# Kernel optimization log

Measured on AMD Instinct MI355X. Metric: run time of the kernel, lower is better.

Reference implementation:

```python
import jax, jax.numpy as jnp
import numpy as np

WIN, SIGMA = 11, 1.5
C1, C2, EPS = 0.01 ** 2, 0.03 ** 2, 1e-8


def _gauss_window(win=WIN, sigma=SIGMA):
    coords = jnp.arange(win, dtype=jnp.float32) - (win - 1) / 2
    g = jnp.exp(-coords ** 2 / (2 * sigma ** 2))
    g = g / g.sum()
    return (g[:, None] * g[None, :])[None, None, :, :]


def setup_inputs() -> dict:
    key = jax.random.key(0)
    k1, k2 = jax.random.split(key)
    N, C, H, W = 32, 1, 512, 512
    x = jax.random.uniform(k1, (N, C, H, W), dtype=jnp.float32)
    y = jax.random.uniform(k2, (N, C, H, W), dtype=jnp.float32)
    w = _gauss_window()
    return {"x": x, "y": y, "w": w}


def _conv(x, w):
    pad = w.shape[-1] // 2
    return jax.lax.conv_general_dilated(
        x, w, window_strides=(1, 1), padding=[(pad, pad), (pad, pad)],
        dimension_numbers=("NCHW", "OIHW", "NCHW"))


def reference(x, y, w):
    w = w.astype(x.dtype)
    n = x.shape[0]
    # One fused conv over all five planes stacked on the batch dim.
    stacked = jnp.concatenate([x, y, x * x, y * y, x * y], axis=0)
    conv = _conv(stacked, w)
    mu_x, mu_y, ex2, ey2, exy = (conv[i * n:(i + 1) * n] for i in range(5))
    mu_x2, mu_y2, mu_xy = mu_x ** 2, mu_y ** 2, mu_x * mu_y
    sig_x2 = ex2 - mu_x2
    sig_y2 = ey2 - mu_y2
    sig_xy = exy - mu_xy
    num = (2 * mu_xy + C1) * (2 * sig_xy + C2)
    den = (mu_x2 + mu_y2 + C1) * (sig_x2 + sig_y2 + C2)
    return jnp.clip(num / (den + EPS), 0.0, 1.0).mean()
```

## Files before the change

### kernel.cpp

```cpp
#include <hip/hip_runtime.h>


typedef float v2f __attribute__((ext_vector_type(2)));
typedef float v4f __attribute__((ext_vector_type(4)));

#define IMG_H 512
#define IMG_W 512
#define NIMG  32
#define NT    256
#define RROWS 32
#define ITERS (RROWS + 10)
#define LDSW  524

#define C1F  1.0e-4f
#define C2F  9.0e-4f
#define EPSF 1.0e-8f

static __device__ __forceinline__ v2f pkfma(float s, v2f a, v2f b) {
    v2f sv = {s, s};
    return __builtin_elementwise_fma(sv, a, b);
}

__global__ __launch_bounds__(NT) void ssim_kernel(
    const float* __restrict__ xg, const float* __restrict__ yg,
    const float* __restrict__ wg, float* __restrict__ out)
{
    const int t    = threadIdx.x;
    const int lane = t & 63;
    const int chnk = blockIdx.x;
    const int img  = blockIdx.y;
    const int r0   = chnk * RROWS;
    const int c0   = 2 * t;

    const float* xb = xg + (size_t)img * (IMG_H * IMG_W);
    const float* yb = yg + (size_t)img * (IMG_H * IMG_W);

    __shared__ alignas(16) v2f ssd[2][LDSW];
    __shared__ float wredS[4];

    float rs = 0.f;
    if (lane < 11) {
        #pragma unroll
        for (int j = 0; j < 11; ++j) rs += wg[lane * 11 + j];
    }
    float g[11];
    #pragma unroll
    for (int k = 0; k < 11; ++k) {
        int gi = __shfl(__float_as_int(rs), k, 64);
        g[k] = __int_as_float(__builtin_amdgcn_readfirstlane(gi));
    }

    const v2f z2 = {0.f, 0.f};

    if (t < 5)        { ssd[0][1 + t]   = z2; ssd[1][1 + t]   = z2; }
    else if (t < 10)  { ssd[0][513 + t] = z2; ssd[1][513 + t] = z2; }

    v2f rSD[11][2], rQ[11][2];

    v2f pfx, pfy;
    {
        const int r = r0 - 5;
        if ((unsigned)r < IMG_H) {
            pfx = *(const v2f*)(xb + (size_t)r * IMG_W + c0);
            pfy = *(const v2f*)(yb + (size_t)r * IMG_W + c0);
        } else { pfx = z2; pfy = z2; }
    }

    float acc = 0.f;

    for (int ii = 0; ii < 44; ii += 11) {
        #pragma unroll
        for (int s = 0; s < 11; ++s) {
            const int i = ii + s;
            if (i < ITERS) {
                const int pb = i & 1;
                {
                    const v2f sv = pfx + pfy;
                    const v2f dv = pfx - pfy;
                    v4f st = {sv.x, dv.x, sv.y, dv.y};
                    *(v4f*)&ssd[pb][6 + c0] = st;
                }
                __syncthreads();

                {
                    const int r = r0 - 4 + i;
                    if ((unsigned)r < IMG_H) {
                        pfx = *(const v2f*)(xb + (size_t)r * IMG_W + c0);
                        pfy = *(const v2f*)(yb + (size_t)r * IMG_W + c0);
                    } else { pfx = z2; pfy = z2; }
                }

                v2f hA = z2, hB = z2, qA = z2, qB = z2;
                #pragma unroll
                for (int m = 0; m < 7; ++m) {
                    const v4f w4 = *(const v4f*)&ssd[pb][c0 + 2 * m];
                    const v2f e0 = {w4.x, w4.y};
                    const v2f e1 = {w4.z, w4.w};
                    {
                        const int j = 2 * m;
                        if (j >= 1) {
                            const v2f f0 = e0 * e0;
                            if (j <= 11) {
                                hA = pkfma(g[j - 1], e0, hA);
                                qA = pkfma(g[j - 1], f0, qA);
                            }
                            if (j >= 2) {
                                hB = pkfma(g[j - 2], e0, hB);
                                qB = pkfma(g[j - 2], f0, qB);
                            }
                        }
                    }
                    {
                        const int j = 2 * m + 1;
                        if (j <= 12) {
                            const v2f f1 = e1 * e1;
                            if (j <= 11) {
                                hA = pkfma(g[j - 1], e1, hA);
                                qA = pkfma(g[j - 1], f1, qA);
                            }
                            if (j >= 2) {
                                hB = pkfma(g[j - 2], e1, hB);
                                qB = pkfma(g[j - 2], f1, qB);
                            }
                        }
                    }
                }
                rSD[s][0] = hA; rSD[s][1] = hB;
                rQ[s][0]  = qA; rQ[s][1]  = qB;

                if (i >= 10) {
                    #pragma unroll
                    for (int c = 0; c < 2; ++c) {
                        v2f mSD = z2, mQ = z2;
                        #pragma unroll
                        for (int j = 0; j < 11; ++j) {
                            const int sl = (s + 1 + j) % 11;
                            mSD = pkfma(g[j], rSD[sl][c], mSD);
                            mQ  = pkfma(g[j], rQ[sl][c],  mQ);
                        }
                        const v2f t2 = mSD * mSD;
                        const float a    = 0.5f  * (t2.x + t2.y);
                        const float muxy = 0.25f * (t2.x - t2.y);
                        const float ep   = 0.5f  * (mQ.x + mQ.y);
                        const float eq   = 0.25f * (mQ.x - mQ.y);
                        const float sxy  = eq - muxy;
                        const float ssum = ep - a;
                        const float num  = fmaf(2.f, muxy, C1F) * fmaf(2.f, sxy, C2F);
                        const float den  = (a + C1F) * (ssum + C2F);
                        float v = num * __builtin_amdgcn_rcpf(den + EPSF);
                        acc += fminf(fmaxf(v, 0.f), 1.f);
                    }
                }
            }
        }
    }

    #pragma unroll
    for (int off = 32; off > 0; off >>= 1)
        acc += __shfl_down(acc, off, 64);
    __syncthreads();
    if (lane == 0) wredS[t >> 6] = acc;
    __syncthreads();
    if (t == 0) {
        const float tot = (wredS[0] + wredS[1]) + (wredS[2] + wredS[3]);
        atomicAdd(out, tot * (1.0f / (float)((size_t)NIMG * IMG_H * IMG_W)));
    }
}

extern "C" void kernel_launch(void* const* d_in, const int* in_sizes, int n_in,
                              void* d_out, int out_size, void* d_ws, size_t ws_size,
                              hipStream_t stream) {
    const float* x = (const float*)d_in[0];
    const float* y = (const float*)d_in[1];
    const float* w = (const float*)d_in[2];
    float* out = (float*)d_out;

    hipMemsetAsync(out, 0, sizeof(float), stream);

    dim3 grid(IMG_H / RROWS, NIMG);
    ssim_kernel<<<grid, dim3(NT), 0, stream>>>(x, y, w, out);
}
```

Baseline: 118.9 us.

## Batch eleven rows per LDS stage to cut block barriers

The LDS staging buffer grows from two rows to eleven. Each thread now loads eleven input rows into registers at once, writes them all to LDS, then runs eleven horizontal/vertical filter steps before the next barrier. This replaces one barrier per row with two per eleven-row chunk and puts more global loads in flight at a time. The cost is more LDS (about 46KB per block), more registers for the prefetched rows, and two extra rows of horizontal filtering whose results are never used.

```diff
diff --git a/kernel.cpp b/kernel.cpp
--- a/kernel.cpp
+++ b/kernel.cpp
@@ -10,6 +10,8 @@
 #define NT    256
 #define RROWS 32
 #define ITERS (RROWS + 10)
+#define CH    11
+#define NCHNK 4
 #define LDSW  524
 
 #define C1F  1.0e-4f
@@ -35,7 +37,7 @@
     const float* xb = xg + (size_t)img * (IMG_H * IMG_W);
     const float* yb = yg + (size_t)img * (IMG_H * IMG_W);
 
-    __shared__ alignas(16) v2f ssd[2][LDSW];
+    __shared__ alignas(16) v2f ssd[CH][LDSW];
     __shared__ float wredS[4];
 
     float rs = 0.f;
@@ -52,113 +54,116 @@
 
     const v2f z2 = {0.f, 0.f};
 
-    if (t < 5)        { ssd[0][1 + t]   = z2; ssd[1][1 + t]   = z2; }
-    else if (t < 10)  { ssd[0][513 + t] = z2; ssd[1][513 + t] = z2; }
+    if (t < 55)               { ssd[t / 5][1 + t % 5] = z2; }
+    if (t >= 128 && t < 183)  { const int u = t - 128; ssd[u / 5][518 + u % 5] = z2; }
 
-    v2f rSD[11][2], rQ[11][2];
+    v2f px[CH], py[CH];
+    #pragma unroll
+    for (int m = 0; m < CH; ++m) {
+        const int r = r0 - 5 + m;
+        if ((unsigned)r < IMG_H) {
+            px[m] = *(const v2f*)(xb + (size_t)r * IMG_W + c0);
+            py[m] = *(const v2f*)(yb + (size_t)r * IMG_W + c0);
+        } else { px[m] = z2; py[m] = z2; }
+    }
 
-    v2f pfx, pfy;
-    {
-        const int r = r0 - 5;
-        if ((unsigned)r < IMG_H) {
-            pfx = *(const v2f*)(xb + (size_t)r * IMG_W + c0);
-            pfy = *(const v2f*)(yb + (size_t)r * IMG_W + c0);
-        } else { pfx = z2; pfy = z2; }
-    }
+    v2f rSD[CH][2], rQ[CH][2];
 
     float acc = 0.f;
 
-    for (int ii = 0; ii < 44; ii += 11) {
+    #pragma unroll 1
+    for (int c = 0; c < NCHNK; ++c) {
         #pragma unroll
-        for (int s = 0; s < 11; ++s) {
-            const int i = ii + s;
-            if (i < ITERS) {
-                const int pb = i & 1;
+        for (int m = 0; m < CH; ++m) {
+            const v2f sv = px[m] + py[m];
+            const v2f dv = px[m] - py[m];
+            v4f st = {sv.x, dv.x, sv.y, dv.y};
+            *(v4f*)&ssd[m][6 + c0] = st;
+        }
+        __syncthreads();
+
+        if (c < NCHNK - 1) {
+            #pragma unroll
+            for (int m = 0; m < CH; ++m) {
+                const int r = r0 + 6 + CH * c + m;
+                if ((unsigned)r < IMG_H) {
+                    px[m] = *(const v2f*)(xb + (size_t)r * IMG_W + c0);
+                    py[m] = *(const v2f*)(yb + (size_t)r * IMG_W + c0);
+                } else { px[m] = z2; py[m] = z2; }
+            }
+        }
+
+        #pragma unroll
+        for (int s = 0; s < CH; ++s) {
+            const int i = CH * c + s;
+            v2f hA = z2, hB = z2, qA = z2, qB = z2;
+            #pragma unroll
+            for (int m = 0; m < 7; ++m) {
+                const v4f w4 = *(const v4f*)&ssd[s][c0 + 2 * m];
+                const v2f e0 = {w4.x, w4.y};
+                const v2f e1 = {w4.z, w4.w};
                 {
-                    const v2f sv = pfx + pfy;
-                    const v2f dv = pfx - pfy;
-                    v4f st = {sv.x, dv.x, sv.y, dv.y};
-                    *(v4f*)&ssd[pb][6 + c0] = st;
-                }
-                __syncthreads();
-
-                {
-                    const int r = r0 - 4 + i;
-                    if ((unsigned)r < IMG_H) {
-                        pfx = *(const v2f*)(xb + (size_t)r * IMG_W + c0);
-                        pfy = *(const v2f*)(yb + (size_t)r * IMG_W + c0);
-                    } else { pfx = z2; pfy = z2; }
-                }
-
-                v2f hA = z2, hB = z2, qA = z2, qB = z2;
-                #pragma unroll
-                for (int m = 0; m < 7; ++m) {
-                    const v4f w4 = *(const v4f*)&ssd[pb][c0 + 2 * m];
-                    const v2f e0 = {w4.x, w4.y};
-                    const v2f e1 = {w4.z, w4.w};
-                    {
-                        const int j = 2 * m;
-                        if (j >= 1) {
-                            const v2f f0 = e0 * e0;
-                            if (j <= 11) {
-                                hA = pkfma(g[j - 1], e0, hA);
-                                qA = pkfma(g[j - 1], f0, qA);
-                            }
-                            if (j >= 2) {
-                                hB = pkfma(g[j - 2], e0, hB);
-                                qB = pkfma(g[j - 2], f0, qB);
-                            }
+                    const int j = 2 * m;
+                    if (j >= 1) {
+                        const v2f f0 = e0 * e0;
+                        if (j <= 11) {
+                            hA = pkfma(g[j - 1], e0, hA);
+                            qA = pkfma(g[j - 1], f0, qA);
                         }
-                    }
-                    {
-                        const int j = 2 * m + 1;
-                        if (j <= 12) {
-                            const v2f f1 = e1 * e1;
-                            if (j <= 11) {
-                                hA = pkfma(g[j - 1], e1, hA);
-                                qA = pkfma(g[j - 1], f1, qA);
-                            }
-                            if (j >= 2) {
-                                hB = pkfma(g[j - 2], e1, hB);
-                                qB = pkfma(g[j - 2], f1, qB);
-                            }
+                        if (j >= 2) {
+                            hB = pkfma(g[j - 2], e0, hB);
+                            qB = pkfma(g[j - 2], f0, qB);
                         }
                     }
                 }
-                rSD[s][0] = hA; rSD[s][1] = hB;
-                rQ[s][0]  = qA; rQ[s][1]  = qB;
-
-                if (i >= 10) {
-                    #pragma unroll
-                    for (int c = 0; c < 2; ++c) {
-                        v2f mSD = z2, mQ = z2;
-                        #pragma unroll
-                        for (int j = 0; j < 11; ++j) {
-                            const int sl = (s + 1 + j) % 11;
-                            mSD = pkfma(g[j], rSD[sl][c], mSD);
-                            mQ  = pkfma(g[j], rQ[sl][c],  mQ);
+                {
+                    const int j = 2 * m + 1;
+                    if (j <= 12) {
+                        const v2f f1 = e1 * e1;
+                        if (j <= 11) {
+                            hA = pkfma(g[j - 1], e1, hA);
+                            qA = pkfma(g[j - 1], f1, qA);
                         }
-                        const v2f t2 = mSD * mSD;
-                        const float a    = 0.5f  * (t2.x + t2.y);
-                        const float muxy = 0.25f * (t2.x - t2.y);
-                        const float ep   = 0.5f  * (mQ.x + mQ.y);
-                        const float eq   = 0.25f * (mQ.x - mQ.y);
-                        const float sxy  = eq - muxy;
-                        const float ssum = ep - a;
-                        const float num  = fmaf(2.f, muxy, C1F) * fmaf(2.f, sxy, C2F);
-                        const float den  = (a + C1F) * (ssum + C2F);
-                        float v = num * __builtin_amdgcn_rcpf(den + EPSF);
-                        acc += fminf(fmaxf(v, 0.f), 1.f);
+                        if (j >= 2) {
+                            hB = pkfma(g[j - 2], e1, hB);
+                            qB = pkfma(g[j - 2], f1, qB);
+                        }
                     }
                 }
             }
+            rSD[s][0] = hA; rSD[s][1] = hB;
+            rQ[s][0]  = qA; rQ[s][1]  = qB;
+
+            if (i >= 10 && i < RROWS + 10) {
+                #pragma unroll
+                for (int cc = 0; cc < 2; ++cc) {
+                    v2f mSD = z2, mQ = z2;
+                    #pragma unroll
+                    for (int j = 0; j < 11; ++j) {
+                        const int sl = (s + 1 + j) % 11;
+                        mSD = pkfma(g[j], rSD[sl][cc], mSD);
+                        mQ  = pkfma(g[j], rQ[sl][cc],  mQ);
+                    }
+                    const v2f t2 = mSD * mSD;
+                    const float a    = 0.5f  * (t2.x + t2.y);
+                    const float muxy = 0.25f * (t2.x - t2.y);
+                    const float ep   = 0.5f  * (mQ.x + mQ.y);
+                    const float eq   = 0.25f * (mQ.x - mQ.y);
+                    const float sxy  = eq - muxy;
+                    const float ssum = ep - a;
+                    const float num  = fmaf(2.f, muxy, C1F) * fmaf(2.f, sxy, C2F);
+                    const float den  = (a + C1F) * (ssum + C2F);
+                    float v = num * __builtin_amdgcn_rcpf(den + EPSF);
+                    acc += fminf(fmaxf(v, 0.f), 1.f);
+                }
+            }
         }
+        __syncthreads();
     }
 
     #pragma unroll
     for (int off = 32; off > 0; off >>= 1)
         acc += __shfl_down(acc, off, 64);
-    __syncthreads();
     if (lane == 0) wredS[t >> 6] = acc;
     __syncthreads();
     if (t == 0) {
```

Result: faster. 116.6 us (-2.0%).
